# Kernel optimization log

Measured on AMD Instinct MI355X. Metric: run time of the kernel, lower is better.

The kernel has to match this reference:

```python
import jax, jax.numpy as jnp
import numpy as np

IN_F = 4096
OUT_F = 11008

def setup_inputs() -> dict:
    key = jax.random.key(0)
    k1, k2, k3, k4 = jax.random.split(key, 4)
    x = jax.random.normal(k1, (4, 128, IN_F), dtype=jnp.float32)
    # int8-style quantized weights stored as int32 in [-127, 127]
    quantized_weight = jax.random.randint(k2, (OUT_F, IN_F), -127, 128, dtype=jnp.int32)
    # per-output-row scale, kept away from zero
    scale = jax.random.uniform(k3, (OUT_F, 1), dtype=jnp.float32, minval=0.5, maxval=1.5)
    bias = jax.random.normal(k4, (OUT_F,), dtype=jnp.float32)
    return {"x": x, "quantized_weight": quantized_weight, "scale": scale, "bias": bias}

def reference(x, quantized_weight, scale, bias):
    # int8 dequantization: weight = q.float() / scale  -> [OUT_F, IN_F] fp32
    weight = quantized_weight.astype(jnp.float32) / scale
    # F.linear(x, weight, bias) == x @ weight.T + bias
    out = jnp.einsum('bsi,oi->bso', x, weight) + bias
    return out
```

## Files before the change

kernel.cpp:

```cpp
#include <hip/hip_runtime.h>
#include <hip/hip_bf16.h>
#include <stdint.h>

#define IN_F  4096
#define OUT_F 11008
#define MTOT  512

#define BM 128
#define BN 64
#define BK 64
#define NKT (IN_F / BK)
#define B_TILE_B (BN * BK * 2)
#define XT_B 16384
#define X_WS_BYTES ((size_t)MTOT * IN_F * 2)

typedef __attribute__((ext_vector_type(4))) float  f32x4;
typedef __attribute__((ext_vector_type(4))) int    i32x4;
typedef __attribute__((ext_vector_type(2))) unsigned u32x2;
typedef __attribute__((ext_vector_type(4))) unsigned u32x4;
typedef __attribute__((ext_vector_type(8))) __bf16 bf16x8;

__device__ __forceinline__ unsigned pack2bf16_rnd(float lo, float hi) {
    unsigned ulo = __builtin_bit_cast(unsigned, lo) + 0x8000u;
    unsigned uhi = __builtin_bit_cast(unsigned, hi) + 0x8000u;
    return __builtin_amdgcn_perm(uhi, ulo, 0x07060302u);
}
__device__ __forceinline__ unsigned pack2bf16_exact(float lo, float hi) {
    return __builtin_amdgcn_perm(__builtin_bit_cast(unsigned, hi),
                                 __builtin_bit_cast(unsigned, lo), 0x07060302u);
}

#define BAR() do {                                                 \
    asm volatile("s_waitcnt lgkmcnt(0)" ::: "memory");             \
    __builtin_amdgcn_s_barrier();                                  \
    __builtin_amdgcn_sched_barrier(0);                             \
} while (0)

__global__ __launch_bounds__(256)
void xconv_kernel(const float* __restrict__ X, char* __restrict__ xws) {
    const int gid  = blockIdx.x * 256 + threadIdx.x;
    const int row  = gid >> 9;
    const int col0 = (gid & 511) * 8;
    const float* src = X + (size_t)row * IN_F + col0;
    f32x4 v0 = *(const f32x4*)(src);
    f32x4 v1 = *(const f32x4*)(src + 4);
    u32x4 o;
    o.x = pack2bf16_rnd(v0.x, v0.y);
    o.y = pack2bf16_rnd(v0.z, v0.w);
    o.z = pack2bf16_rnd(v1.x, v1.y);
    o.w = pack2bf16_rnd(v1.z, v1.w);
    const int mtile = row >> 7, mrow = row & 127;
    const int mi = mrow >> 4,  l15 = mrow & 15;
    const int kt  = col0 >> 6;
    const int ks  = (col0 >> 5) & 1;
    const int lhi = (col0 >> 3) & 3;
    const int lane = lhi * 16 + l15;
    const int f = mi * 2 + ks;
    *(u32x4*)(xws + ((size_t)(mtile * NKT + kt) * 16 + f) * 1024
                  + lane * 16) = o;
}

__global__ __launch_bounds__(128, 2)
void qgemm_kernel(const char* __restrict__ xws,
                  const int*   __restrict__ W,
                  const float* __restrict__ scale,
                  const float* __restrict__ bias,
                  float* __restrict__ Out)
{
    __shared__ __align__(16) char smem[2 * B_TILE_B];
    char* bufB0 = smem;
    char* bufB1 = smem + B_TILE_B;

    const int tid  = (int)threadIdx.x;
    const int lane = tid & 63;
    const int w    = tid >> 6;

    const int bid = (int)blockIdx.x;
    const int xcd = bid & 7;
    const int j   = bid >> 3;
    const int mtile = (xcd & 1) * 2 + (j & 1);
    const int ntile = (xcd >> 1) * 43 + (j >> 1);
    const int brow = mtile * BM;
    const int bcol = ntile * BN;

    const int srow  = tid >> 4;
    const int scol4 = tid & 15;
    const int* Wp = W + (size_t)(bcol + srow) * IN_F + scol4 * 4;

    const char* xAw = xws + (size_t)mtile * (NKT * XT_B) + w * 8192 + lane * 16;

    i32x4 rb[8];
    bf16x8 afE[8], afO[8];
    f32x4 acc[4][4];
    #pragma unroll
    for (int i = 0; i < 4; ++i)
        #pragma unroll
        for (int jj = 0; jj < 4; ++jj)
            acc[i][jj] = (f32x4){0.f, 0.f, 0.f, 0.f};

    #define LOAD_A(AF, KT)                                                   \
        _Pragma("unroll")                                                    \
        for (int q = 0; q < 8; ++q)                                          \
            AF[q] = *(const bf16x8*)(xAw + (size_t)(KT) * XT_B + q * 1024);

    #define LOAD_B(KT)                                                       \
        _Pragma("unroll")                                                    \
        for (int k = 0; k < 8; ++k)                                          \
            rb[k] = *(const i32x4*)(Wp + (size_t)(KT) * BK                   \
                                       + (size_t)(k * 8) * IN_F);

    #define CONVERT_B(DSTB)                                                  \
        _Pragma("unroll")                                                    \
        for (int k = 0; k < 8; ++k) {                                        \
            const int row = srow + k * 8;                                    \
            const int off = (row * 128 + scol4 * 8) ^ ((row & 7) << 4);      \
            u32x2 bv;                                                        \
            bv.x = pack2bf16_exact((float)rb[k].x, (float)rb[k].y);          \
            bv.y = pack2bf16_exact((float)rb[k].z, (float)rb[k].w);          \
            *(u32x2*)((DSTB) + off) = bv;                                    \
        }

    #define MFMA_PHASE(AF, BUFB)                                             \
        _Pragma("unroll")                                                    \
        for (int ks = 0; ks < 2; ++ks) {                                     \
            bf16x8 bfr[4];                                                   \
            _Pragma("unroll")                                                \
            for (int ni = 0; ni < 4; ++ni) {                                 \
                const int row = ni * 16 + (lane & 15);                       \
                const int off = (row * 128 + ks * 64 + (lane >> 4) * 16)     \
                                ^ ((row & 7) << 4);                          \
                bfr[ni] = *(const bf16x8*)((BUFB) + off);                    \
            }                                                                \
            __builtin_amdgcn_s_setprio(1);                                   \
            _Pragma("unroll")                                                \
            for (int mi = 0; mi < 4; ++mi)                                   \
                _Pragma("unroll")                                            \
                for (int ni = 0; ni < 4; ++ni)                               \
                    acc[mi][ni] = __builtin_amdgcn_mfma_f32_16x16x32_bf16(   \
                        AF[mi * 2 + ks], bfr[ni], acc[mi][ni], 0, 0, 0);     \
            __builtin_amdgcn_s_setprio(0);                                   \
        }

    LOAD_B(0);
    CONVERT_B(bufB0);
    LOAD_A(afE, 0);
    LOAD_B(1);
    BAR();

    for (int kt2 = 0; kt2 < NKT; kt2 += 2) {
        const bool last = (kt2 == NKT - 2);

        LOAD_A(afO, kt2 + 1);
        CONVERT_B(bufB1);
        if (!last) LOAD_B(kt2 + 2);
        MFMA_PHASE(afE, bufB0);
        BAR();

        if (!last) {
            LOAD_A(afE, kt2 + 2);
            CONVERT_B(bufB0);
            LOAD_B(kt2 + 3);
        }
        MFMA_PHASE(afO, bufB1);
        if (!last) BAR();
    }

    #pragma unroll
    for (int ni = 0; ni < 4; ++ni) {
        const int col = bcol + ni * 16 + (lane & 15);
        const float inv = 1.0f / scale[col];
        const float bs  = bias[col];
        #pragma unroll
        for (int mi = 0; mi < 4; ++mi) {
            const int row0 = brow + w * 64 + mi * 16 + ((lane >> 4) << 2);
            #pragma unroll
            for (int jj = 0; jj < 4; ++jj)
                Out[(size_t)(row0 + jj) * OUT_F + col] = acc[mi][ni][jj] * inv + bs;
        }
    }

    #undef LOAD_A
    #undef LOAD_B
    #undef CONVERT_B
    #undef MFMA_PHASE
}

__global__ __launch_bounds__(128, 2)
void qgemm_fallback_kernel(const float* __restrict__ X,
                           const int*   __restrict__ W,
                           const float* __restrict__ scale,
                           const float* __restrict__ bias,
                           float* __restrict__ Out)
{
    __shared__ __align__(16) char smem[BM * BK * 2 + B_TILE_B];
    char* bufA = smem;
    char* bufB = smem + BM * BK * 2;

    const int tid  = (int)threadIdx.x;
    const int lane = tid & 63;
    const int w    = tid >> 6;

    const int bid  = (int)blockIdx.x;
    const int lbid = (bid & 7) * 86 + (bid >> 3);
    const int mtile = lbid & 3;
    const int ntile = lbid >> 2;
    const int brow = mtile * BM;
    const int bcol = ntile * BN;

    const int srow  = tid >> 4;
    const int scol4 = tid & 15;
    const int* Wp = W + (size_t)(bcol + srow) * IN_F + scol4 * 4;
    const float* Xp = X + (size_t)(brow + srow) * IN_F + scol4 * 4;

    f32x4 acc[4][4];
    #pragma unroll
    for (int i = 0; i < 4; ++i)
        #pragma unroll
        for (int jj = 0; jj < 4; ++jj)
            acc[i][jj] = (f32x4){0.f, 0.f, 0.f, 0.f};

    for (int kt = 0; kt < NKT; ++kt) {
        #pragma unroll
        for (int k = 0; k < 8; ++k) {
            i32x4 rb = *(const i32x4*)(Wp + (size_t)kt * BK + (size_t)(k * 8) * IN_F);
            const int row = srow + k * 8;
            const int off = (row * 128 + scol4 * 8) ^ ((row & 7) << 4);
            u32x2 bv;
            bv.x = pack2bf16_exact((float)rb.x, (float)rb.y);
            bv.y = pack2bf16_exact((float)rb.z, (float)rb.w);
            *(u32x2*)(bufB + off) = bv;
        }
        #pragma unroll
        for (int k = 0; k < 16; ++k) {
            f32x4 ra = *(const f32x4*)(Xp + (size_t)kt * BK + (size_t)(k * 8) * IN_F);
            const int row = srow + k * 8;
            const int off = (row * 128 + scol4 * 8) ^ ((row & 7) << 4);
            u32x2 av;
            av.x = pack2bf16_rnd(ra.x, ra.y);
            av.y = pack2bf16_rnd(ra.z, ra.w);
            *(u32x2*)(bufA + off) = av;
        }
        __syncthreads();
        #pragma unroll
        for (int ks = 0; ks < 2; ++ks) {
            bf16x8 af[4], bfr[4];
            #pragma unroll
            for (int mi = 0; mi < 4; ++mi) {
                const int row = w * 64 + mi * 16 + (lane & 15);
                const int off = (row * 128 + ks * 64 + (lane >> 4) * 16)
                                ^ ((row & 7) << 4);
                af[mi] = *(const bf16x8*)(bufA + off);
            }
            #pragma unroll
            for (int ni = 0; ni < 4; ++ni) {
                const int row = ni * 16 + (lane & 15);
                const int off = (row * 128 + ks * 64 + (lane >> 4) * 16)
                                ^ ((row & 7) << 4);
                bfr[ni] = *(const bf16x8*)(bufB + off);
            }
            #pragma unroll
            for (int mi = 0; mi < 4; ++mi)
                #pragma unroll
                for (int ni = 0; ni < 4; ++ni)
                    acc[mi][ni] = __builtin_amdgcn_mfma_f32_16x16x32_bf16(
                        af[mi], bfr[ni], acc[mi][ni], 0, 0, 0);
        }
        __syncthreads();
    }

    #pragma unroll
    for (int ni = 0; ni < 4; ++ni) {
        const int col = bcol + ni * 16 + (lane & 15);
        const float inv = 1.0f / scale[col];
        const float bs  = bias[col];
        #pragma unroll
        for (int mi = 0; mi < 4; ++mi) {
            const int row0 = brow + w * 64 + mi * 16 + ((lane >> 4) << 2);
            #pragma unroll
            for (int jj = 0; jj < 4; ++jj)
                Out[(size_t)(row0 + jj) * OUT_F + col] = acc[mi][ni][jj] * inv + bs;
        }
    }
}

extern "C" void kernel_launch(void* const* d_in, const int* in_sizes, int n_in,
                              void* d_out, int out_size, void* d_ws, size_t ws_size,
                              hipStream_t stream) {
    const float* X     = (const float*)d_in[0];
    const int*   W     = (const int*)d_in[1];
    const float* scale = (const float*)d_in[2];
    const float* bias  = (const float*)d_in[3];
    float* Out = (float*)d_out;

    const int grid = (MTOT / BM) * (OUT_F / BN);

    if (ws_size >= X_WS_BYTES) {
        char* xws = (char*)d_ws;
        xconv_kernel<<<(MTOT * IN_F / 8) / 256, 256, 0, stream>>>(X, xws);
        qgemm_kernel<<<grid, 128, 0, stream>>>(xws, W, scale, bias, Out);
    } else {
        qgemm_fallback_kernel<<<grid, 128, 0, stream>>>(X, W, scale, bias, Out);
    }
}
```

Measured before the change: 81.52 us.

## Deepen W prefetch to two tiles ahead and remap block-to-tile order

Adds a second register buffer for the int32 weight tile so global loads of W are issued two k-tiles ahead of their conversion. A-fragment loads move to after each MFMA phase. This is meant to hide more global-memory latency behind compute. The block-index to tile mapping also changes so each XCD gets a contiguous range of linear tile ids, with the 4 m-tiles of an n-tile adjacent, which may improve L2 reuse of W. The cost is 32 more VGPRs for the second weight buffer, which could hurt occupancy under launch_bounds(128,2) or cause spills.

```diff
diff --git a/kernel.cpp b/kernel.cpp
--- a/kernel.cpp
+++ b/kernel.cpp
@@ -75,11 +75,10 @@
     const int lane = tid & 63;
     const int w    = tid >> 6;
 
-    const int bid = (int)blockIdx.x;
-    const int xcd = bid & 7;
-    const int j   = bid >> 3;
-    const int mtile = (xcd & 1) * 2 + (j & 1);
-    const int ntile = (xcd >> 1) * 43 + (j >> 1);
+    const int bid  = (int)blockIdx.x;
+    const int lbid = (bid & 7) * 86 + (bid >> 3);
+    const int mtile = lbid & 3;
+    const int ntile = lbid >> 2;
     const int brow = mtile * BM;
     const int bcol = ntile * BN;
 
@@ -89,7 +88,7 @@
 
     const char* xAw = xws + (size_t)mtile * (NKT * XT_B) + w * 8192 + lane * 16;
 
-    i32x4 rb[8];
+    i32x4 rbE[8], rbO[8];
     bf16x8 afE[8], afO[8];
     f32x4 acc[4][4];
     #pragma unroll
@@ -103,20 +102,20 @@
         for (int q = 0; q < 8; ++q)                                          \
             AF[q] = *(const bf16x8*)(xAw + (size_t)(KT) * XT_B + q * 1024);
 
-    #define LOAD_B(KT)                                                       \
+    #define LOAD_B(RB, KT)                                                   \
         _Pragma("unroll")                                                    \
         for (int k = 0; k < 8; ++k)                                          \
-            rb[k] = *(const i32x4*)(Wp + (size_t)(KT) * BK                   \
+            RB[k] = *(const i32x4*)(Wp + (size_t)(KT) * BK                   \
                                        + (size_t)(k * 8) * IN_F);
 
-    #define CONVERT_B(DSTB)                                                  \
+    #define CONVERT_B(RB, DSTB)                                              \
         _Pragma("unroll")                                                    \
         for (int k = 0; k < 8; ++k) {                                        \
             const int row = srow + k * 8;                                    \
             const int off = (row * 128 + scol4 * 8) ^ ((row & 7) << 4);      \
             u32x2 bv;                                                        \
-            bv.x = pack2bf16_exact((float)rb[k].x, (float)rb[k].y);          \
-            bv.y = pack2bf16_exact((float)rb[k].z, (float)rb[k].w);          \
+            bv.x = pack2bf16_exact((float)RB[k].x, (float)RB[k].y);          \
+            bv.y = pack2bf16_exact((float)RB[k].z, (float)RB[k].w);          \
             *(u32x2*)((DSTB) + off) = bv;                                    \
         }
 
@@ -141,28 +140,28 @@
             __builtin_amdgcn_s_setprio(0);                                   \
         }
 
-    LOAD_B(0);
-    CONVERT_B(bufB0);
+    LOAD_B(rbE, 0);
+    CONVERT_B(rbE, bufB0);
+    LOAD_B(rbO, 1);
+    LOAD_B(rbE, 2);
     LOAD_A(afE, 0);
-    LOAD_B(1);
+    LOAD_A(afO, 1);
     BAR();
 
     for (int kt2 = 0; kt2 < NKT; kt2 += 2) {
-        const bool last = (kt2 == NKT - 2);
-
-        LOAD_A(afO, kt2 + 1);
-        CONVERT_B(bufB1);
-        if (!last) LOAD_B(kt2 + 2);
+        CONVERT_B(rbO, bufB1);
+        if (kt2 + 3 < NKT) LOAD_B(rbO, kt2 + 3);
         MFMA_PHASE(afE, bufB0);
+        if (kt2 + 2 < NKT) LOAD_A(afE, kt2 + 2);
         BAR();
 
-        if (!last) {
-            LOAD_A(afE, kt2 + 2);
-            CONVERT_B(bufB0);
-            LOAD_B(kt2 + 3);
+        if (kt2 + 2 < NKT) {
+            CONVERT_B(rbE, bufB0);
+            if (kt2 + 4 < NKT) LOAD_B(rbE, kt2 + 4);
         }
         MFMA_PHASE(afO, bufB1);
-        if (!last) BAR();
+        if (kt2 + 3 < NKT) LOAD_A(afO, kt2 + 3);
+        if (kt2 + 2 < NKT) BAR();
     }
 
     #pragma unroll
```

After: 99.61 us. +22.2%, slower.

## Enlarge GEMM block tile to 256x128 with 8 waves in a 4x2 grid

Applied to the files above, without the earlier changes.

The main quantized GEMM kernel moves from a 128x64 tile with 2 waves to a 256x128 tile with 8 waves (512 threads), arranged as 4 waves along M and 2 along N. Each int32 weight tile converted to bf16 in LDS is now reused by more rows of X, which cuts redundant global weight reads and conversions. The block-to-tile mapping is reworked for 172 blocks spread over XCDs, and the s_setprio hints around the MFMAs are removed. The grid shrinks to 172 blocks on a GPU with more CUs than that, so some CUs sit idle and per-block register pressure rises.

```diff
diff --git a/kernel.cpp b/kernel.cpp
--- a/kernel.cpp
+++ b/kernel.cpp
@@ -6,8 +6,8 @@
 #define OUT_F 11008
 #define MTOT  512
 
-#define BM 128
-#define BN 64
+#define BM 256
+#define BN 128
 #define BK 64
 #define NKT (IN_F / BK)
 #define B_TILE_B (BN * BK * 2)
@@ -49,18 +49,18 @@
     o.y = pack2bf16_rnd(v0.z, v0.w);
     o.z = pack2bf16_rnd(v1.x, v1.y);
     o.w = pack2bf16_rnd(v1.z, v1.w);
-    const int mtile = row >> 7, mrow = row & 127;
+    const int xmt = row >> 7, mrow = row & 127;
     const int mi = mrow >> 4,  l15 = mrow & 15;
     const int kt  = col0 >> 6;
     const int ks  = (col0 >> 5) & 1;
     const int lhi = (col0 >> 3) & 3;
     const int lane = lhi * 16 + l15;
     const int f = mi * 2 + ks;
-    *(u32x4*)(xws + ((size_t)(mtile * NKT + kt) * 16 + f) * 1024
+    *(u32x4*)(xws + ((size_t)(xmt * NKT + kt) * 16 + f) * 1024
                   + lane * 16) = o;
 }
 
-__global__ __launch_bounds__(128, 2)
+__global__ __launch_bounds__(512, 2)
 void qgemm_kernel(const char* __restrict__ xws,
                   const int*   __restrict__ W,
                   const float* __restrict__ scale,
@@ -73,23 +73,27 @@
 
     const int tid  = (int)threadIdx.x;
     const int lane = tid & 63;
-    const int w    = tid >> 6;
+    const int wid  = tid >> 6;
+    const int wm   = wid >> 1;
+    const int wn   = wid & 1;
 
     const int bid = (int)blockIdx.x;
     const int xcd = bid & 7;
     const int j   = bid >> 3;
-    const int mtile = (xcd & 1) * 2 + (j & 1);
-    const int ntile = (xcd >> 1) * 43 + (j >> 1);
-    const int brow = mtile * BM;
+    const int lbid = (xcd < 4) ? (xcd * 22 + j) : (88 + (xcd - 4) * 21 + j);
+    const int mt  = lbid & 1;
+    const int ntile = lbid >> 1;
+    const int brow = mt * BM;
     const int bcol = ntile * BN;
 
     const int srow  = tid >> 4;
     const int scol4 = tid & 15;
     const int* Wp = W + (size_t)(bcol + srow) * IN_F + scol4 * 4;
 
-    const char* xAw = xws + (size_t)mtile * (NKT * XT_B) + w * 8192 + lane * 16;
-
-    i32x4 rb[8];
+    const char* xAw = xws + (size_t)(2 * mt + (wm >> 1)) * (NKT * XT_B)
+                    + (wm & 1) * 8192 + lane * 16;
+
+    i32x4 rb[4];
     bf16x8 afE[8], afO[8];
     f32x4 acc[4][4];
     #pragma unroll
@@ -105,14 +109,14 @@
 
     #define LOAD_B(KT)                                                       \
         _Pragma("unroll")                                                    \
-        for (int k = 0; k < 8; ++k)                                          \
+        for (int k = 0; k < 4; ++k)                                          \
             rb[k] = *(const i32x4*)(Wp + (size_t)(KT) * BK                   \
-                                       + (size_t)(k * 8) * IN_F);
+                                       + (size_t)(k * 32) * IN_F);
 
     #define CONVERT_B(DSTB)                                                  \
         _Pragma("unroll")                                                    \
-        for (int k = 0; k < 8; ++k) {                                        \
-            const int row = srow + k * 8;                                    \
+        for (int k = 0; k < 4; ++k) {                                        \
+            const int row = srow + k * 32;                                   \
             const int off = (row * 128 + scol4 * 8) ^ ((row & 7) << 4);      \
             u32x2 bv;                                                        \
             bv.x = pack2bf16_exact((float)rb[k].x, (float)rb[k].y);          \
@@ -126,19 +130,17 @@
             bf16x8 bfr[4];                                                   \
             _Pragma("unroll")                                                \
             for (int ni = 0; ni < 4; ++ni) {                                 \
-                const int row = ni * 16 + (lane & 15);                       \
+                const int row = wn * 64 + ni * 16 + (lane & 15);             \
                 const int off = (row * 128 + ks * 64 + (lane >> 4) * 16)     \
                                 ^ ((row & 7) << 4);                          \
                 bfr[ni] = *(const bf16x8*)((BUFB) + off);                    \
             }                                                                \
-            __builtin_amdgcn_s_setprio(1);                                   \
             _Pragma("unroll")                                                \
             for (int mi = 0; mi < 4; ++mi)                                   \
                 _Pragma("unroll")                                            \
                 for (int ni = 0; ni < 4; ++ni)                               \
                     acc[mi][ni] = __builtin_amdgcn_mfma_f32_16x16x32_bf16(   \
                         AF[mi * 2 + ks], bfr[ni], acc[mi][ni], 0, 0, 0);     \
-            __builtin_amdgcn_s_setprio(0);                                   \
         }
 
     LOAD_B(0);
@@ -167,12 +169,12 @@
 
     #pragma unroll
     for (int ni = 0; ni < 4; ++ni) {
-        const int col = bcol + ni * 16 + (lane & 15);
+        const int col = bcol + wn * 64 + ni * 16 + (lane & 15);
         const float inv = 1.0f / scale[col];
         const float bs  = bias[col];
         #pragma unroll
         for (int mi = 0; mi < 4; ++mi) {
-            const int row0 = brow + w * 64 + mi * 16 + ((lane >> 4) << 2);
+            const int row0 = brow + wm * 64 + mi * 16 + ((lane >> 4) << 2);
             #pragma unroll
             for (int jj = 0; jj < 4; ++jj)
                 Out[(size_t)(row0 + jj) * OUT_F + col] = acc[mi][ni][jj] * inv + bs;
@@ -192,9 +194,9 @@
                            const float* __restrict__ bias,
                            float* __restrict__ Out)
 {
-    __shared__ __align__(16) char smem[BM * BK * 2 + B_TILE_B];
+    __shared__ __align__(16) char smem[128 * BK * 2 + 64 * BK * 2];
     char* bufA = smem;
-    char* bufB = smem + BM * BK * 2;
+    char* bufB = smem + 128 * BK * 2;
 
     const int tid  = (int)threadIdx.x;
     const int lane = tid & 63;
@@ -204,8 +206,8 @@
     const int lbid = (bid & 7) * 86 + (bid >> 3);
     const int mtile = lbid & 3;
     const int ntile = lbid >> 2;
-    const int brow = mtile * BM;
-    const int bcol = ntile * BN;
+    const int brow = mtile * 128;
+    const int bcol = ntile * 64;
 
     const int srow  = tid >> 4;
     const int scol4 = tid & 15;
@@ -292,13 +294,13 @@
     const float* bias  = (const float*)d_in[3];
     float* Out = (float*)d_out;
 
-    const int grid = (MTOT / BM) * (OUT_F / BN);
-
     if (ws_size >= X_WS_BYTES) {
         char* xws = (char*)d_ws;
         xconv_kernel<<<(MTOT * IN_F / 8) / 256, 256, 0, stream>>>(X, xws);
-        qgemm_kernel<<<grid, 128, 0, stream>>>(xws, W, scale, bias, Out);
+        const int grid = (MTOT / BM) * (OUT_F / BN);
+        qgemm_kernel<<<grid, 512, 0, stream>>>(xws, W, scale, bias, Out);
     } else {
+        const int grid = 688;
         qgemm_fallback_kernel<<<grid, 128, 0, stream>>>(X, W, scale, bias, Out);
     }
 }
```

After: 87.95 us. 1.08x slower.

## Quantize activations per row to int8 and use int8 MFMA

Applied to the files above, without the earlier changes.

The activation prep kernel now computes a per-row absmax scale and quantizes x to int8 instead of bf16. The GEMM packs the int32 weights into int8 in LDS and accumulates with the 16x16x64 int8 MFMA, then rescales in the epilogue by the row scale times the inverse weight scale. This halves the A-operand and LDS traffic, removes the float conversion of weights, and uses the higher-throughput int8 matrix path. It also changes the block-to-tile mapping and reorders the MFMA, convert and load steps. The cost is extra quantization error on the activations compared with bf16, which may threaten the accuracy tolerance.

```diff
diff --git a/kernel.cpp b/kernel.cpp
--- a/kernel.cpp
+++ b/kernel.cpp
@@ -10,9 +10,10 @@
 #define BN 64
 #define BK 64
 #define NKT (IN_F / BK)
-#define B_TILE_B (BN * BK * 2)
-#define XT_B 16384
-#define X_WS_BYTES ((size_t)MTOT * IN_F * 2)
+#define B_TILE_B (BN * BK)
+#define XT_B 8192
+#define SX_OFF ((size_t)MTOT * IN_F)
+#define X_WS_BYTES (SX_OFF + MTOT * 4)
 
 typedef __attribute__((ext_vector_type(4))) float  f32x4;
 typedef __attribute__((ext_vector_type(4))) int    i32x4;
@@ -29,6 +30,11 @@
     return __builtin_amdgcn_perm(__builtin_bit_cast(unsigned, hi),
                                  __builtin_bit_cast(unsigned, lo), 0x07060302u);
 }
+__device__ __forceinline__ unsigned pack4_i8(i32x4 v) {
+    unsigned r1 = __builtin_amdgcn_perm((unsigned)v.y, (unsigned)v.x, 0x00000400u);
+    unsigned r2 = __builtin_amdgcn_perm((unsigned)v.w, (unsigned)v.z, 0x00000400u);
+    return __builtin_amdgcn_perm(r2, r1, 0x05040100u);
+}
 
 #define BAR() do {                                                 \
     asm volatile("s_waitcnt lgkmcnt(0)" ::: "memory");             \
@@ -37,31 +43,56 @@
 } while (0)
 
 __global__ __launch_bounds__(256)
-void xconv_kernel(const float* __restrict__ X, char* __restrict__ xws) {
-    const int gid  = blockIdx.x * 256 + threadIdx.x;
-    const int row  = gid >> 9;
-    const int col0 = (gid & 511) * 8;
-    const float* src = X + (size_t)row * IN_F + col0;
+void xconv_kernel(const float* __restrict__ X, char* __restrict__ xws,
+                  float* __restrict__ sx) {
+    const int row = (int)blockIdx.x;
+    const int t   = (int)threadIdx.x;
+    const float* src = X + (size_t)row * IN_F + t * 16;
     f32x4 v0 = *(const f32x4*)(src);
     f32x4 v1 = *(const f32x4*)(src + 4);
+    f32x4 v2 = *(const f32x4*)(src + 8);
+    f32x4 v3 = *(const f32x4*)(src + 12);
+
+    float m = 0.f;
+    #pragma unroll
+    for (int i = 0; i < 4; ++i) {
+        m = fmaxf(m, fmaxf(fmaxf(fabsf(v0[i]), fabsf(v1[i])),
+                           fmaxf(fabsf(v2[i]), fabsf(v3[i]))));
+    }
+    #pragma unroll
+    for (int off = 32; off >= 1; off >>= 1)
+        m = fmaxf(m, __shfl_xor(m, off));
+    __shared__ float red[4];
+    if ((t & 63) == 0) red[t >> 6] = m;
+    __syncthreads();
+    m = fmaxf(fmaxf(red[0], red[1]), fmaxf(red[2], red[3]));
+    m = fmaxf(m, 1e-20f);
+    const float inv = 127.0f / m;
+    if (t == 0) sx[row] = m * (1.0f / 127.0f);
+
+    i32x4 q0, q1, q2, q3;
+    #pragma unroll
+    for (int i = 0; i < 4; ++i) {
+        q0[i] = (int)__builtin_rintf(v0[i] * inv);
+        q1[i] = (int)__builtin_rintf(v1[i] * inv);
+        q2[i] = (int)__builtin_rintf(v2[i] * inv);
+        q3[i] = (int)__builtin_rintf(v3[i] * inv);
+    }
     u32x4 o;
-    o.x = pack2bf16_rnd(v0.x, v0.y);
-    o.y = pack2bf16_rnd(v0.z, v0.w);
-    o.z = pack2bf16_rnd(v1.x, v1.y);
-    o.w = pack2bf16_rnd(v1.z, v1.w);
+    o.x = pack4_i8(q0); o.y = pack4_i8(q1);
+    o.z = pack4_i8(q2); o.w = pack4_i8(q3);
+
     const int mtile = row >> 7, mrow = row & 127;
-    const int mi = mrow >> 4,  l15 = mrow & 15;
-    const int kt  = col0 >> 6;
-    const int ks  = (col0 >> 5) & 1;
-    const int lhi = (col0 >> 3) & 3;
-    const int lane = lhi * 16 + l15;
-    const int f = mi * 2 + ks;
-    *(u32x4*)(xws + ((size_t)(mtile * NKT + kt) * 16 + f) * 1024
+    const int f = mrow >> 4, l15 = mrow & 15;
+    const int kt = t >> 2;
+    const int h  = t & 3;
+    const int lane = h * 16 + l15;
+    *(u32x4*)(xws + ((size_t)(mtile * NKT + kt)) * XT_B + f * 1024
                   + lane * 16) = o;
 }
 
 __global__ __launch_bounds__(128, 2)
-void qgemm_kernel(const char* __restrict__ xws,
+void qgemm_kernel(const char* __restrict__ xws, const float* __restrict__ sx,
                   const int*   __restrict__ W,
                   const float* __restrict__ scale,
                   const float* __restrict__ bias,
@@ -75,94 +106,91 @@
     const int lane = tid & 63;
     const int w    = tid >> 6;
 
-    const int bid = (int)blockIdx.x;
-    const int xcd = bid & 7;
-    const int j   = bid >> 3;
-    const int mtile = (xcd & 1) * 2 + (j & 1);
-    const int ntile = (xcd >> 1) * 43 + (j >> 1);
+    const int bid  = (int)blockIdx.x;
+    const int lbid = (bid & 7) * 86 + (bid >> 3);
+    const int mtile = lbid & 3;
+    const int ntile = lbid >> 2;
     const int brow = mtile * BM;
     const int bcol = ntile * BN;
 
-    const int srow  = tid >> 4;
-    const int scol4 = tid & 15;
-    const int* Wp = W + (size_t)(bcol + srow) * IN_F + scol4 * 4;
-
-    const char* xAw = xws + (size_t)mtile * (NKT * XT_B) + w * 8192 + lane * 16;
+    const int f1 = tid >> 6;
+    const int l1 = tid & 63;
+    const int r1 = bcol + f1 * 16 + (l1 & 15);
+    const int kw = (l1 >> 4) * 16;
+    const int* Wp1 = W + (size_t)r1 * IN_F + kw;
+    const int* Wp2 = Wp1 + (size_t)32 * IN_F;
+
+    const char* xA = xws + (size_t)mtile * (NKT * XT_B) + (w * 4) * 1024
+                   + lane * 16;
 
     i32x4 rb[8];
-    bf16x8 afE[8], afO[8];
-    f32x4 acc[4][4];
+    i32x4 afE[4], afO[4];
+    i32x4 acc[4][4];
     #pragma unroll
     for (int i = 0; i < 4; ++i)
         #pragma unroll
         for (int jj = 0; jj < 4; ++jj)
-            acc[i][jj] = (f32x4){0.f, 0.f, 0.f, 0.f};
+            acc[i][jj] = (i32x4){0, 0, 0, 0};
 
     #define LOAD_A(AF, KT)                                                   \
         _Pragma("unroll")                                                    \
-        for (int q = 0; q < 8; ++q)                                          \
-            AF[q] = *(const bf16x8*)(xAw + (size_t)(KT) * XT_B + q * 1024);
+        for (int mi = 0; mi < 4; ++mi)                                       \
+            AF[mi] = *(const i32x4*)(xA + (size_t)(KT) * XT_B + mi * 1024);
 
     #define LOAD_B(KT)                                                       \
         _Pragma("unroll")                                                    \
-        for (int k = 0; k < 8; ++k)                                          \
-            rb[k] = *(const i32x4*)(Wp + (size_t)(KT) * BK                   \
-                                       + (size_t)(k * 8) * IN_F);
+        for (int k = 0; k < 4; ++k) {                                        \
+            rb[k]     = *(const i32x4*)(Wp1 + (size_t)(KT) * BK + k * 4);    \
+            rb[k + 4] = *(const i32x4*)(Wp2 + (size_t)(KT) * BK + k * 4);    \
+        }
 
     #define CONVERT_B(DSTB)                                                  \
-        _Pragma("unroll")                                                    \
-        for (int k = 0; k < 8; ++k) {                                        \
-            const int row = srow + k * 8;                                    \
-            const int off = (row * 128 + scol4 * 8) ^ ((row & 7) << 4);      \
-            u32x2 bv;                                                        \
-            bv.x = pack2bf16_exact((float)rb[k].x, (float)rb[k].y);          \
-            bv.y = pack2bf16_exact((float)rb[k].z, (float)rb[k].w);          \
-            *(u32x2*)((DSTB) + off) = bv;                                    \
-        }
+        do {                                                                 \
+            u32x4 o1, o2;                                                    \
+            o1.x = pack4_i8(rb[0]); o1.y = pack4_i8(rb[1]);                  \
+            o1.z = pack4_i8(rb[2]); o1.w = pack4_i8(rb[3]);                  \
+            o2.x = pack4_i8(rb[4]); o2.y = pack4_i8(rb[5]);                  \
+            o2.z = pack4_i8(rb[6]); o2.w = pack4_i8(rb[7]);                  \
+            *(u32x4*)((DSTB) + tid * 16) = o1;                               \
+            *(u32x4*)((DSTB) + tid * 16 + 2048) = o2;                        \
+        } while (0)
 
     #define MFMA_PHASE(AF, BUFB)                                             \
-        _Pragma("unroll")                                                    \
-        for (int ks = 0; ks < 2; ++ks) {                                     \
-            bf16x8 bfr[4];                                                   \
+        do {                                                                 \
+            i32x4 bfr[4];                                                    \
             _Pragma("unroll")                                                \
-            for (int ni = 0; ni < 4; ++ni) {                                 \
-                const int row = ni * 16 + (lane & 15);                       \
-                const int off = (row * 128 + ks * 64 + (lane >> 4) * 16)     \
-                                ^ ((row & 7) << 4);                          \
-                bfr[ni] = *(const bf16x8*)((BUFB) + off);                    \
-            }                                                                \
-            __builtin_amdgcn_s_setprio(1);                                   \
+            for (int ni = 0; ni < 4; ++ni)                                   \
+                bfr[ni] = *(const i32x4*)((BUFB) + ni * 1024 + lane * 16);   \
             _Pragma("unroll")                                                \
             for (int mi = 0; mi < 4; ++mi)                                   \
                 _Pragma("unroll")                                            \
                 for (int ni = 0; ni < 4; ++ni)                               \
-                    acc[mi][ni] = __builtin_amdgcn_mfma_f32_16x16x32_bf16(   \
-                        AF[mi * 2 + ks], bfr[ni], acc[mi][ni], 0, 0, 0);     \
-            __builtin_amdgcn_s_setprio(0);                                   \
-        }
+                    acc[mi][ni] = __builtin_amdgcn_mfma_i32_16x16x64_i8(     \
+                        AF[mi], bfr[ni], acc[mi][ni], 0, 0, 0);              \
+        } while (0)
 
     LOAD_B(0);
     CONVERT_B(bufB0);
+    LOAD_B(1);
     LOAD_A(afE, 0);
-    LOAD_B(1);
     BAR();
 
     for (int kt2 = 0; kt2 < NKT; kt2 += 2) {
-        const bool last = (kt2 == NKT - 2);
+        const bool more = (kt2 + 2 < NKT);
 
         LOAD_A(afO, kt2 + 1);
+        MFMA_PHASE(afE, bufB0);
         CONVERT_B(bufB1);
-        if (!last) LOAD_B(kt2 + 2);
-        MFMA_PHASE(afE, bufB0);
+        if (more) LOAD_B(kt2 + 2);
         BAR();
 
-        if (!last) {
-            LOAD_A(afE, kt2 + 2);
+        if (more) LOAD_A(afE, kt2 + 2);
+        MFMA_PHASE(afO, bufB1);
+        if (more) {
             CONVERT_B(bufB0);
-            LOAD_B(kt2 + 3);
-        }
-        MFMA_PHASE(afO, bufB1);
-        if (!last) BAR();
+            if (kt2 + 3 < NKT) LOAD_B(kt2 + 3);
+            BAR();
+        }
     }
 
     #pragma unroll
@@ -173,9 +201,11 @@
         #pragma unroll
         for (int mi = 0; mi < 4; ++mi) {
             const int row0 = brow + w * 64 + mi * 16 + ((lane >> 4) << 2);
+            const f32x4 sxq = *(const f32x4*)(sx + row0);
             #pragma unroll
             for (int jj = 0; jj < 4; ++jj)
-                Out[(size_t)(row0 + jj) * OUT_F + col] = acc[mi][ni][jj] * inv + bs;
+                Out[(size_t)(row0 + jj) * OUT_F + col] =
+                    (float)acc[mi][ni][jj] * (sxq[jj] * inv) + bs;
         }
     }
 
@@ -192,7 +222,7 @@
                            const float* __restrict__ bias,
                            float* __restrict__ Out)
 {
-    __shared__ __align__(16) char smem[BM * BK * 2 + B_TILE_B];
+    __shared__ __align__(16) char smem[BM * BK * 2 + BN * BK * 2];
     char* bufA = smem;
     char* bufB = smem + BM * BK * 2;
 
@@ -295,9 +325,10 @@
     const int grid = (MTOT / BM) * (OUT_F / BN);
 
     if (ws_size >= X_WS_BYTES) {
-        char* xws = (char*)d_ws;
-        xconv_kernel<<<(MTOT * IN_F / 8) / 256, 256, 0, stream>>>(X, xws);
-        qgemm_kernel<<<grid, 128, 0, stream>>>(xws, W, scale, bias, Out);
+        char*  xws = (char*)d_ws;
+        float* sx  = (float*)((char*)d_ws + SX_OFF);
+        xconv_kernel<<<MTOT, 256, 0, stream>>>(X, xws, sx);
+        qgemm_kernel<<<grid, 128, 0, stream>>>(xws, sx, W, scale, bias, Out);
     } else {
         qgemm_fallback_kernel<<<grid, 128, 0, stream>>>(X, W, scale, bias, Out);
     }
```

Measured after the change: 110.6 us. 1.36x slower.
